# Kernel tuning notes

Measured on AMD Instinct MI355X. Metric: run time of the kernel, lower is better.

Reference implementation:

```python
import jax, jax.numpy as jnp
import numpy as np

B_, L_, D_ = 8, 2048, 1024
ED = 2 * D_          # d_inner (expand=2)
N_ = D_ // 16        # d_state = 64
R_ = -(-D_ // 16)    # dt_rank = ceil(d_model/16) = 64
K_ = 4               # d_conv
NL = 3               # number of mamba layers
NC = 2               # num_classes
STD = 0.02


def setup_inputs() -> dict:
    key = jax.random.key(0)
    ks = jax.random.split(key, 8)
    # Standard Mamba init: A_log = log(1..N) broadcast over channels
    A_log = jnp.log(jnp.tile(jnp.arange(1, N_ + 1, dtype=jnp.float32), (NL, ED, 1)))
    return {
        "x": jax.random.normal(ks[0], (B_, L_, D_), jnp.float32),
        "W_in": jax.random.normal(ks[1], (NL, 2 * ED, D_), jnp.float32) * STD,
        "conv_w": jax.random.normal(ks[2], (NL, ED, 1, K_), jnp.float32) * STD,
        "conv_b": jnp.zeros((NL, ED), jnp.float32),
        "W_x": jax.random.normal(ks[3], (NL, R_ + 2 * N_, ED), jnp.float32) * STD,
        "W_dt": jax.random.normal(ks[4], (NL, ED, R_), jnp.float32) * STD,
        "b_dt": jnp.zeros((NL, ED), jnp.float32),
        "A_log": A_log,
        "D_p": jnp.ones((NL, ED), jnp.float32),
        "W_out": jax.random.normal(ks[5], (NL, D_, ED), jnp.float32) * STD,
        "norm_w": jnp.ones((NL, D_), jnp.float32),
        "W_head": jax.random.normal(ks[6], (NC, D_), jnp.float32) * STD,
        "b_head": jnp.zeros((NC,), jnp.float32),
    }


def _silu(x):
    return x * jax.nn.sigmoid(x)


def _rmsnorm(x, w, eps=1e-5):
    return x * jax.lax.rsqrt(jnp.mean(x * x, axis=-1, keepdims=True) + eps) * w


def _mamba_block(x, Wi, cw, cb, Wx, Wdt, bdt, Alog, Dp, Wo):
    B, L, D = x.shape
    xz = x @ Wi.T                              # (B, L, 2*ED)
    xp, z = jnp.split(xz, 2, axis=-1)          # each (B, L, ED)
    # causal depthwise conv1d (kernel K_, left-pad K_-1)
    xc = jnp.transpose(xp, (0, 2, 1))          # (B, ED, L)
    xc = jax.lax.conv_general_dilated(
        xc, cw, window_strides=(1,), padding=[(K_ - 1, 0)],
        dimension_numbers=("NCH", "OIH", "NCH"), feature_group_count=ED,
    ) + cb[None, :, None]
    xp = _silu(jnp.transpose(xc, (0, 2, 1)))   # (B, L, ED)

    xdbl = xp @ Wx.T                           # (B, L, R + 2N)
    dt, Bm, Cm = jnp.split(xdbl, [R_, R_ + N_], axis=-1)
    delta = jax.nn.softplus(dt @ Wdt.T + bdt)  # (B, L, ED)
    A = -jnp.exp(Alog)                         # (ED, N)

    def step(h, inp):
        d_t, B_t, C_t, x_t = inp               # (B,ED), (B,N), (B,N), (B,ED)
        h = jnp.exp(d_t[..., None] * A) * h + (d_t * x_t)[..., None] * B_t[:, None, :]
        y_t = jnp.einsum("ben,bn->be", h, C_t)
        return h, y_t

    h0 = jnp.zeros((B, ED, N_), x.dtype)
    xs = (jnp.moveaxis(delta, 1, 0), jnp.moveaxis(Bm, 1, 0),
          jnp.moveaxis(Cm, 1, 0), jnp.moveaxis(xp, 1, 0))
    _, ys = jax.lax.scan(step, h0, xs)         # ys: (L, B, ED)
    y = jnp.moveaxis(ys, 0, 1) + xp * Dp       # (B, L, ED)
    y = y * _silu(z)
    return y @ Wo.T                            # (B, L, D)


def reference(x, W_in, conv_w, conv_b, W_x, W_dt, b_dt, A_log, D_p, W_out,
              norm_w, W_head, b_head):
    for i in range(NL):
        z = _mamba_block(x, W_in[i], conv_w[i], conv_b[i], W_x[i], W_dt[i],
                         b_dt[i], A_log[i], D_p[i], W_out[i])
        x = _rmsnorm(z, norm_w[i]) + x         # dropout_rate=0 -> identity
    last = x[:, -1, :]                         # (B, D)
    return last @ W_head.T + b_head            # (B, NC)
```

## Files before the change

### kernel.cpp

```cpp
#include <hip/hip_runtime.h>
#include <math.h>

#define B_ 8
#define L_ 2048
#define D_ 1024
#define ED_ 2048
#define NL_ 3
#define NC_ 2
#define SCH_ 128
#define NCH_ (L_ / SCH_)
#define GSZ_ 16
#define NGR_ (SCH_ / GSZ_)

typedef unsigned short u16;
typedef unsigned int u32;
typedef __attribute__((ext_vector_type(8))) short short8;
typedef __attribute__((ext_vector_type(4))) float f32x4;

#define LOG2E_ 1.44269504088896f

__device__ __forceinline__ u16 f2b(float f) {
    u32 u = __float_as_uint(f);
    u = (u + 0x7FFFu + ((u >> 16) & 1u)) >> 16;
    return (u16)u;
}
__device__ __forceinline__ float b2f(u16 h) {
    return __uint_as_float(((u32)h) << 16);
}
__device__ __forceinline__ float fexp2(float x) {
#if __has_builtin(__builtin_amdgcn_exp2f)
    return __builtin_amdgcn_exp2f(x);
#else
    return exp2f(x);
#endif
}
__device__ __forceinline__ void cp16(const void* g, void* l) {
    __builtin_amdgcn_global_load_lds((const __attribute__((address_space(1))) u32*)g,
                                     (__attribute__((address_space(3))) u32*)l,
                                     16, 0, 0);
}

__global__ __launch_bounds__(256)
void cast_bf16(const float* __restrict__ in, u16* __restrict__ out, int n)
{
    int i = blockIdx.x * 256 + threadIdx.x;
    if (i < n) out[i] = f2b(in[i]);
}

__global__ __launch_bounds__(256)
void cast_dt(const float* __restrict__ xdbl, u16* __restrict__ dtb)
{
    int idx = blockIdx.x * 256 + threadIdx.x;
    int m = idx >> 6, r = idx & 63;
    dtb[idx] = f2b(xdbl[(size_t)m * 192 + r]);
}

template<int BM, int BN, int EPI>
__global__ __launch_bounds__(256)
void gemm_mfma(const u16* __restrict__ A, int lda,
               const u16* __restrict__ W, const float* __restrict__ bias,
               void* __restrict__ Cout, int ldc, int Kd)
{
    constexpr int WX = (BN == 128) ? 2 : ((BM == 128) ? 1 : 2);
    constexpr int WY = 4 / WX;
    constexpr int MI = (BM / WY) / 16;
    constexpr int NI = (BN / WX) / 16;

    __shared__ u16 As[BM * 32];
    __shared__ u16 Bs[BN * 32];

    const int tid  = threadIdx.x;
    const int wave = tid >> 6;
    const int lane = tid & 63;
    const int wy = wave / WX, wx = wave % WX;
    const int by = blockIdx.y * BM;
    const int bx = blockIdx.x * BN;
    const int lr = lane & 15;
    const int lk = (lane >> 4) * 8;

    f32x4 acc[MI][NI];
#pragma unroll
    for (int i = 0; i < MI; i++)
#pragma unroll
        for (int j = 0; j < NI; j++) acc[i][j] = (f32x4){0.f, 0.f, 0.f, 0.f};

    const u16* Ag0 = A + (size_t)(by + (tid >> 2)) * lda + (tid & 3) * 8;
    const u16* Bg0 = W + (size_t)(bx + (tid >> 2)) * Kd + (tid & 3) * 8;
    u16* ldsA0 = &As[wave * 512];
    u16* ldsB0 = &Bs[wave * 512];

    for (int kt = 0; kt < Kd; kt += 32) {
        __syncthreads();
        cp16(Ag0 + kt, ldsA0);
        if (BM == 128) cp16(Ag0 + (size_t)64 * lda + kt, ldsA0 + 2048);
        cp16(Bg0 + kt, ldsB0);
        if (BN == 128) cp16(Bg0 + (size_t)64 * Kd + kt, ldsB0 + 2048);
        __syncthreads();

        short8 af[MI], bf[NI];
#pragma unroll
        for (int mi = 0; mi < MI; mi++) {
            int m = wy * (MI * 16) + mi * 16 + lr;
            af[mi] = *(const short8*)&As[m * 32 + lk];
        }
#pragma unroll
        for (int ni = 0; ni < NI; ni++) {
            int n = wx * (NI * 16) + ni * 16 + lr;
            bf[ni] = *(const short8*)&Bs[n * 32 + lk];
        }
#pragma unroll
        for (int mi = 0; mi < MI; mi++)
#pragma unroll
            for (int ni = 0; ni < NI; ni++)
                acc[mi][ni] = __builtin_amdgcn_mfma_f32_16x16x32_bf16(
                    af[mi], bf[ni], acc[mi][ni], 0, 0, 0);
    }

#pragma unroll
    for (int mi = 0; mi < MI; mi++) {
#pragma unroll
        for (int ni = 0; ni < NI; ni++) {
            int col = bx + wx * (NI * 16) + ni * 16 + lr;
#pragma unroll
            for (int r = 0; r < 4; r++) {
                int row = by + wy * (MI * 16) + mi * 16 + (lane >> 4) * 4 + r;
                float v = acc[mi][ni][r];
                if (EPI == 2) {
                    v += bias[col];
                    v = (v > 20.f) ? v : log1pf(__expf(v));
                }
                if (EPI == 1)
                    ((u16*)Cout)[(size_t)row * ldc + col] = f2b(v);
                else
                    ((float*)Cout)[(size_t)row * ldc + col] = v;
            }
        }
    }
}

__global__ __launch_bounds__(256)
void conv_silu(const u16* __restrict__ xzb, const float* __restrict__ cw,
               const float* __restrict__ cb, u16* __restrict__ xpb)
{
    int idx = blockIdx.x * 256 + threadIdx.x;
    int e = idx & (ED_ - 1);
    int l = (idx >> 11) & (L_ - 1);
    int b = idx >> 22;
    const float w0 = cw[e * 4 + 0], w1 = cw[e * 4 + 1];
    const float w2 = cw[e * 4 + 2], w3 = cw[e * 4 + 3];
    const u16* base = xzb + (size_t)(b * L_) * 4096 + e;
    float x0 = (l >= 3) ? b2f(base[(size_t)(l - 3) * 4096]) : 0.f;
    float x1 = (l >= 2) ? b2f(base[(size_t)(l - 2) * 4096]) : 0.f;
    float x2 = (l >= 1) ? b2f(base[(size_t)(l - 1) * 4096]) : 0.f;
    float x3 = b2f(base[(size_t)l * 4096]);
    float v = cb[e] + w0 * x0 + w1 * x1 + w2 * x2 + w3 * x3;
    v = v / (1.f + __expf(-v));
    xpb[idx] = f2b(v);
}

struct SlotP { const char* p; int st; };

__device__ __forceinline__ SlotP p1_slot(int s, const float* xdbl, const float* delta,
                                         const u16* xpb, size_t rowBase, int e0)
{
    SlotP r;
    if (s < 256) {
        int l = s >> 4, f = (s & 15) * 4;
        r.p = (const char*)(xdbl + (rowBase + l) * 192 + 64 + f);
        r.st = 16 * 192 * 4;
    } else if (s < 384) {
        int ss = s - 256; int l = ss >> 3, f = (ss & 7) * 4;
        r.p = (const char*)(delta + (rowBase + l) * 2048 + e0 + f);
        r.st = 16 * 2048 * 4;
    } else {
        int ss = s - 384; int l = ss >> 2, q = ss & 3;
        r.p = (const char*)(xpb + (rowBase + l) * 2048 + e0 + q * 8);
        r.st = 16 * 2048 * 2;
    }
    return r;
}

__global__ __launch_bounds__(512)
void scan_pass1(const float* __restrict__ delta, const float* __restrict__ xdbl,
                const u16* __restrict__ xpb, const float* __restrict__ A_log,
                float* __restrict__ hbuf, float* __restrict__ sumd)
{
    __shared__ __align__(16) char arena[2][7168];

    const int tid = threadIdx.x;
    const int wv = tid >> 6, ln = tid & 63;
    const int c = tid >> 4, j = tid & 15;
    const int b = blockIdx.z, ch = blockIdx.y;
    const int e0 = blockIdx.x << 5;
    const int e = e0 + c;
    const int l0 = ch * SCH_;
    const size_t rowBase = (size_t)(b * L_) + l0;

    const int s0 = wv * 56 + ln;
    SlotP sp0 = p1_slot(ln < 56 ? s0 : 0, xdbl, delta, xpb, rowBase, e0);
    const int d0 = s0 * 16;

    auto stage = [&](int gi) {
        char* a = (char*)arena[gi & 1];
        if (ln < 56) { cp16(sp0.p, a + d0); sp0.p += sp0.st; }
    };

    stage(0);

    float4 Al = *(const float4*)(A_log + (size_t)e * 64 + 4 * j);
    const float A0 = -__expf(Al.x) * LOG2E_, A1 = -__expf(Al.y) * LOG2E_;
    const float A2 = -__expf(Al.z) * LOG2E_, A3 = -__expf(Al.w) * LOG2E_;

    float h0 = 0.f, h1 = 0.f, h2 = 0.f, h3 = 0.f, sd = 0.f;

    for (int g = 0; g < NGR_; ++g) {
        if (g + 1 < NGR_) {
            stage(g + 1);
            asm volatile("s_waitcnt vmcnt(1)" ::: "memory");
        } else {
            asm volatile("s_waitcnt vmcnt(0)" ::: "memory");
        }
        __builtin_amdgcn_s_barrier();
        const char* bufp = (const char*)arena[g & 1];
#pragma unroll
        for (int t = 0; t < GSZ_; ++t) {
            float  dv = *(const float*)(bufp + 4096 + t * 128 + c * 4);
            float  xv = b2f(*(const u16*)(bufp + 6144 + t * 64 + c * 2));
            float4 Bv = *(const float4*)(bufp + t * 256 + j * 16);
            float dx = dv * xv;
            h0 = fexp2(dv * A0) * h0 + dx * Bv.x;
            h1 = fexp2(dv * A1) * h1 + dx * Bv.y;
            h2 = fexp2(dv * A2) * h2 + dx * Bv.z;
            h3 = fexp2(dv * A3) * h3 + dx * Bv.w;
            sd += dv;
        }
        __builtin_amdgcn_s_barrier();
    }

    size_t slot = (((size_t)(b * NCH_ + ch) * ED_) + e) * 64 + 4 * j;
    *(float4*)(hbuf + slot) = make_float4(h0, h1, h2, h3);
    if (j == 0) sumd[(size_t)(b * NCH_ + ch) * ED_ + e] = sd;
}

__global__ __launch_bounds__(256)
void scan_pass2(float* __restrict__ hbuf, const float* __restrict__ sumd,
                const float* __restrict__ A_log)
{
    int idx = blockIdx.x * 256 + threadIdx.x;
    int n = idx & 63;
    int e = (idx >> 6) & (ED_ - 1);
    int b = idx >> 17;
    float A = -__expf(A_log[e * 64 + n]) * LOG2E_;
    float h = 0.f;
#pragma unroll
    for (int c = 0; c < NCH_; ++c) {
        size_t slot = (((size_t)(b * NCH_ + c) * ED_) + e) * 64 + n;
        float v = 0.f, sd = 0.f;
        if (c < NCH_ - 1) {
            v  = hbuf[slot];
            sd = sumd[(size_t)(b * NCH_ + c) * ED_ + e];
        }
        hbuf[slot] = h;
        if (c < NCH_ - 1) h = fexp2(A * sd) * h + v;
    }
}

__device__ __forceinline__ SlotP p3_slot(int s, const float* xdbl, const float* delta,
                                         const u16* xpb, const u16* xzb,
                                         size_t rowBase, int e0)
{
    SlotP r;
    if (s < 512) {
        int cc = s >> 8;
        int l = (s >> 4) & 15, f = (s & 15) * 4;
        r.p = (const char*)(xdbl + (rowBase + l) * 192 + 64 + cc * 64 + f);
        r.st = 16 * 192 * 4;
    } else if (s < 640) {
        int ss = s - 512; int l = ss >> 3, f = (ss & 7) * 4;
        r.p = (const char*)(delta + (rowBase + l) * 2048 + e0 + f);
        r.st = 16 * 2048 * 4;
    } else if (s < 704) {
        int ss = s - 640; int l = ss >> 2, q = ss & 3;
        r.p = (const char*)(xpb + (rowBase + l) * 2048 + e0 + q * 8);
        r.st = 16 * 2048 * 2;
    } else {
        int ss = s - 704; int l = ss >> 2, q = ss & 3;
        r.p = (const char*)(xzb + (rowBase + l) * 4096 + 2048 + e0 + q * 8);
        r.st = 16 * 4096 * 2;
    }
    return r;
}

__global__ __launch_bounds__(512)
void scan_pass3(const float* __restrict__ delta, const float* __restrict__ xdbl,
                const u16* __restrict__ xzb, u16* __restrict__ xpb,
                const float* __restrict__ A_log, const float* __restrict__ Dp,
                const float* __restrict__ hbuf)
{
    __shared__ __align__(16) char arena[2][12288];

    const int tid = threadIdx.x;
    const int wv = tid >> 6, ln = tid & 63;
    const int c = tid >> 4, j = tid & 15;
    const int b = blockIdx.z, ch = blockIdx.y;
    const int e0 = blockIdx.x << 5;
    const int e = e0 + c;
    const int l0 = ch * SCH_;
    const size_t rowBase = (size_t)(b * L_) + l0;

    const int s0 = wv * 96 + ln;
    SlotP sp0 = p3_slot(s0, xdbl, delta, xpb, xzb, rowBase, e0);
    SlotP sp1 = p3_slot(ln < 32 ? s0 + 64 : s0, xdbl, delta, xpb, xzb, rowBase, e0);
    const int d0 = s0 * 16, d1 = d0 + 1024;

    auto stage = [&](int gi) {
        char* a = (char*)arena[gi & 1];
        cp16(sp0.p, a + d0); sp0.p += sp0.st;
        if (ln < 32) { cp16(sp1.p, a + d1); sp1.p += sp1.st; }
    };

    stage(0);

    float4 Al = *(const float4*)(A_log + (size_t)e * 64 + 4 * j);
    const float A0 = -__expf(Al.x) * LOG2E_, A1 = -__expf(Al.y) * LOG2E_;
    const float A2 = -__expf(Al.z) * LOG2E_, A3 = -__expf(Al.w) * LOG2E_;
    const float dpe = Dp[e];

    size_t slot = (((size_t)(b * NCH_ + ch) * ED_) + e) * 64 + 4 * j;
    float4 hi = *(const float4*)(hbuf + slot);
    float h0 = hi.x, h1 = hi.y, h2 = hi.z, h3 = hi.w;

    for (int g = 0; g < NGR_; ++g) {
        if (g + 1 < NGR_) {
            stage(g + 1);
            asm volatile("s_waitcnt vmcnt(2)" ::: "memory");
        } else {
            asm volatile("s_waitcnt vmcnt(0)" ::: "memory");
        }
        __builtin_amdgcn_s_barrier();
        const char* bufp = (const char*)arena[g & 1];

        float yreg = 0.f;
#pragma unroll
        for (int t = 0; t < GSZ_; ++t) {
            float  dv = *(const float*)(bufp + 8192 + t * 128 + c * 4);
            float  xv = b2f(*(const u16*)(bufp + 10240 + t * 64 + c * 2));
            float4 Bv = *(const float4*)(bufp + t * 256 + j * 16);
            float4 Cv = *(const float4*)(bufp + 4096 + t * 256 + j * 16);
            float dx = dv * xv;
            h0 = fexp2(dv * A0) * h0 + dx * Bv.x;
            h1 = fexp2(dv * A1) * h1 + dx * Bv.y;
            h2 = fexp2(dv * A2) * h2 + dx * Bv.z;
            h3 = fexp2(dv * A3) * h3 + dx * Bv.w;

            float acc = h0 * Cv.x + h1 * Cv.y + h2 * Cv.z + h3 * Cv.w;
            acc += __shfl_xor(acc, 1); acc += __shfl_xor(acc, 2);
            acc += __shfl_xor(acc, 4); acc += __shfl_xor(acc, 8);
            float yv = acc + xv * dpe;
            if (j == t) yreg = yv;
        }
        {
            float zv = b2f(*(const u16*)(bufp + 11264 + j * 64 + c * 2));
            float sz = zv / (1.f + __expf(-zv));
            xpb[(rowBase + g * 16 + j) * 2048 + e] = f2b(yreg * sz);
        }
        __builtin_amdgcn_s_barrier();
    }
}

__global__ __launch_bounds__(256)
void rmsnorm_res(const float* __restrict__ t, const float* __restrict__ nw,
                 float* __restrict__ x, u16* __restrict__ xb)
{
    const int row = blockIdx.x;
    const int tid = threadIdx.x;
    const float* tr = t + (size_t)row * D_;
    float* xr = x + (size_t)row * D_;
    u16* xbr = xb + (size_t)row * D_;
    float4 v = *(const float4*)(tr + tid * 4);
    float ss = v.x * v.x + v.y * v.y + v.z * v.z + v.w * v.w;
#pragma unroll
    for (int m = 1; m < 64; m <<= 1) ss += __shfl_xor(ss, m);
    __shared__ float red[4];
    if ((tid & 63) == 0) red[tid >> 6] = ss;
    __syncthreads();
    float tot = red[0] + red[1] + red[2] + red[3];
    float scale = rsqrtf(tot * (1.f / (float)D_) + 1e-5f);
    float4 w = *(const float4*)(nw + tid * 4);
    float4 xo = *(const float4*)(xr + tid * 4);
    xo.x += v.x * scale * w.x;
    xo.y += v.y * scale * w.y;
    xo.z += v.z * scale * w.z;
    xo.w += v.w * scale * w.w;
    *(float4*)(xr + tid * 4) = xo;
    ushort4 hb;
    hb.x = f2b(xo.x); hb.y = f2b(xo.y); hb.z = f2b(xo.z); hb.w = f2b(xo.w);
    *(ushort4*)(xbr + tid * 4) = hb;
}

__global__ __launch_bounds__(256)
void head_kernel(const float* __restrict__ x, const float* __restrict__ Wh,
                 const float* __restrict__ bh, float* __restrict__ out)
{
    const int b = blockIdx.x >> 1, c = blockIdx.x & 1;
    const int tid = threadIdx.x;
    const float* xr = x + (size_t)(b * L_ + (L_ - 1)) * D_;
    const float* wr = Wh + c * D_;
    float4 xv = *(const float4*)(xr + tid * 4);
    float4 wv = *(const float4*)(wr + tid * 4);
    float s = xv.x * wv.x + xv.y * wv.y + xv.z * wv.z + xv.w * wv.w;
#pragma unroll
    for (int m = 1; m < 64; m <<= 1) s += __shfl_xor(s, m);
    __shared__ float red[4];
    if ((tid & 63) == 0) red[tid >> 6] = s;
    __syncthreads();
    if (tid == 0) out[b * 2 + c] = red[0] + red[1] + red[2] + red[3] + bh[c];
}

extern "C" void kernel_launch(void* const* d_in, const int* in_sizes, int n_in,
                              void* d_out, int out_size, void* d_ws, size_t ws_size,
                              hipStream_t stream)
{
    const float* x_in   = (const float*)d_in[0];
    const float* W_in   = (const float*)d_in[1];
    const float* conv_w = (const float*)d_in[2];
    const float* conv_b = (const float*)d_in[3];
    const float* W_x    = (const float*)d_in[4];
    const float* W_dt   = (const float*)d_in[5];
    const float* b_dt   = (const float*)d_in[6];
    const float* A_log  = (const float*)d_in[7];
    const float* D_p    = (const float*)d_in[8];
    const float* W_out  = (const float*)d_in[9];
    const float* norm_w = (const float*)d_in[10];
    const float* W_head = (const float*)d_in[11];
    const float* b_head = (const float*)d_in[12];
    float* out = (float*)d_out;

    const size_t nWi = (size_t)NL_ * 2 * ED_ * D_;
    const size_t nWx = (size_t)NL_ * 192 * ED_;
    const size_t nWo = (size_t)NL_ * D_ * ED_;
    const size_t nWd = (size_t)NL_ * ED_ * 64;
    u16* Wi_b = (u16*)d_ws;
    u16* Wx_b = Wi_b + nWi;
    u16* Wo_b = Wx_b + nWx;
    u16* Wd_b = Wo_b + nWo;
    size_t wbytes = ((nWi + nWx + nWo + nWd) * 2 + 255) & ~(size_t)255;
    char* gb = (char*)d_ws + wbytes;
    size_t usable = ws_size - wbytes;

    cast_bf16<<<(int)(nWi / 256), 256, 0, stream>>>(W_in, Wi_b, (int)nWi);
    cast_bf16<<<(int)(nWx / 256), 256, 0, stream>>>(W_x,  Wx_b, (int)nWx);
    cast_bf16<<<(int)(nWo / 256), 256, 0, stream>>>(W_out, Wo_b, (int)nWo);
    cast_bf16<<<(int)(nWd / 256), 256, 0, stream>>>(W_dt,  Wd_b, (int)nWd);

    const size_t perB = (size_t)L_ * (D_ * 4 + 192 * 4 + ED_ * 4 + 4096 * 2 + ED_ * 2)
                      + (size_t)NCH_ * ED_ * 64 * 4 + (size_t)NCH_ * ED_ * 4
                      + (size_t)L_ * 64 * 2;
    int G = 8;
    while (G > 1 && (size_t)G * perB > usable) G >>= 1;
    const int M = G * L_;

    float* x_cur = (float*)gb;
    float* xdbl  = x_cur + (size_t)M * D_;
    float* delta = xdbl + (size_t)M * 192;
    u16*   x_b   = (u16*)delta;
    u16*   xz_b  = (u16*)(delta + (size_t)M * ED_);
    u16*   xps_b = xz_b + (size_t)M * 4096;
    float* hbuf  = (float*)(xps_b + (size_t)M * ED_);
    float* sumd  = hbuf + (size_t)G * NCH_ * ED_ * 64;
    u16*   dtb   = (u16*)(sumd + (size_t)G * NCH_ * ED_);
    float* out_t = (float*)xz_b;

    for (int g0 = 0; g0 < B_; g0 += G) {
        const float* xg = x_in + (size_t)g0 * L_ * D_;
        hipMemcpyAsync(x_cur, xg, (size_t)M * D_ * sizeof(float),
                       hipMemcpyDeviceToDevice, stream);
        cast_bf16<<<(M * D_) / 256, 256, 0, stream>>>(xg, x_b, M * D_);

        for (int i = 0; i < NL_; ++i) {
            gemm_mfma<128, 128, 1><<<dim3(4096 / 128, M / 128), 256, 0, stream>>>(
                x_b, D_, Wi_b + (size_t)i * 2 * ED_ * D_, nullptr, xz_b, 4096, D_);
            conv_silu<<<(M * ED_) / 256, 256, 0, stream>>>(
                xz_b, conv_w + (size_t)i * ED_ * 4, conv_b + (size_t)i * ED_, xps_b);
            gemm_mfma<64, 64, 0><<<dim3(192 / 64, M / 64), 256, 0, stream>>>(
                xps_b, ED_, Wx_b + (size_t)i * 192 * ED_, nullptr, xdbl, 192, ED_);
            cast_dt<<<(M * 64) / 256, 256, 0, stream>>>(xdbl, dtb);
            gemm_mfma<64, 64, 2><<<dim3(ED_ / 64, M / 64), 256, 0, stream>>>(
                dtb, 64, Wd_b + (size_t)i * ED_ * 64, b_dt + (size_t)i * ED_,
                delta, ED_, 64);
            scan_pass1<<<dim3(ED_ / 32, NCH_ - 1, G), 512, 0, stream>>>(
                delta, xdbl, xps_b, A_log + (size_t)i * ED_ * 64, hbuf, sumd);
            scan_pass2<<<G * 512, 256, 0, stream>>>(
                hbuf, sumd, A_log + (size_t)i * ED_ * 64);
            scan_pass3<<<dim3(ED_ / 32, NCH_, G), 512, 0, stream>>>(
                delta, xdbl, xz_b, xps_b,
                A_log + (size_t)i * ED_ * 64, D_p + (size_t)i * ED_, hbuf);
            gemm_mfma<64, 128, 0><<<dim3(D_ / 128, M / 64), 256, 0, stream>>>(
                xps_b, ED_, Wo_b + (size_t)i * D_ * ED_, nullptr, out_t, D_, ED_);
            rmsnorm_res<<<M, 256, 0, stream>>>(out_t, norm_w + (size_t)i * D_,
                                               x_cur, x_b);
        }
        head_kernel<<<G * NC_, 256, 0, stream>>>(x_cur, W_head, b_head,
                                                 out + (size_t)g0 * NC_);
    }
}
```

Baseline: 5.230 ms.

## Pack delta, x and z into interleaved 8-byte records; batch y reduction in scan

The delta GEMM epilogue now writes one 8-byte record per (row, channel) holding fp32 delta plus the bf16 x and z values, so both scan passes stage a single contiguous stream instead of three strided ones. In pass 3 the per-timestep 16-lane shuffle reduction of C·h is replaced by a recursive-halving transpose-reduce over a 16-element register array, which cuts the shuffle count. The cost is an extra read of xps and xz in the GEMM epilogue, a larger delta buffer, and more registers held in pass 3.

Result: faster. 4.661 ms (-10.9%).

```diff
diff --git a/kernel.cpp b/kernel.cpp
--- a/kernel.cpp
+++ b/kernel.cpp
@@ -59,7 +59,8 @@
 __global__ __launch_bounds__(256)
 void gemm_mfma(const u16* __restrict__ A, int lda,
                const u16* __restrict__ W, const float* __restrict__ bias,
-               void* __restrict__ Cout, int ldc, int Kd)
+               void* __restrict__ Cout, int ldc, int Kd,
+               const u16* __restrict__ xq, const u16* __restrict__ zq)
 {
     constexpr int WX = (BN == 128) ? 2 : ((BM == 128) ? 1 : 2);
     constexpr int WY = 4 / WX;
@@ -128,11 +129,17 @@
                 if (EPI == 2) {
                     v += bias[col];
                     v = (v > 20.f) ? v : log1pf(__expf(v));
+                    u16 xv = xq[(size_t)row * ED_ + col];
+                    u16 zv = zq[(size_t)row * 4096 + 2048 + col];
+                    uint2 pkv;
+                    pkv.x = __float_as_uint(v);
+                    pkv.y = (u32)xv | ((u32)zv << 16);
+                    ((uint2*)Cout)[(size_t)row * ldc + col] = pkv;
+                } else if (EPI == 1) {
+                    ((u16*)Cout)[(size_t)row * ldc + col] = f2b(v);
+                } else {
+                    ((float*)Cout)[(size_t)row * ldc + col] = v;
                 }
-                if (EPI == 1)
-                    ((u16*)Cout)[(size_t)row * ldc + col] = f2b(v);
-                else
-                    ((float*)Cout)[(size_t)row * ldc + col] = v;
             }
         }
     }
@@ -160,32 +167,28 @@
 
 struct SlotP { const char* p; int st; };
 
-__device__ __forceinline__ SlotP p1_slot(int s, const float* xdbl, const float* delta,
-                                         const u16* xpb, size_t rowBase, int e0)
+__device__ __forceinline__ SlotP p1_slot(int s, const float* xdbl, const char* pkc,
+                                         size_t rowBase, int e0)
 {
     SlotP r;
     if (s < 256) {
         int l = s >> 4, f = (s & 15) * 4;
         r.p = (const char*)(xdbl + (rowBase + l) * 192 + 64 + f);
         r.st = 16 * 192 * 4;
-    } else if (s < 384) {
-        int ss = s - 256; int l = ss >> 3, f = (ss & 7) * 4;
-        r.p = (const char*)(delta + (rowBase + l) * 2048 + e0 + f);
-        r.st = 16 * 2048 * 4;
     } else {
-        int ss = s - 384; int l = ss >> 2, q = ss & 3;
-        r.p = (const char*)(xpb + (rowBase + l) * 2048 + e0 + q * 8);
-        r.st = 16 * 2048 * 2;
+        int ss = s - 256; int l = ss >> 4, f = (ss & 15) * 16;
+        r.p = pkc + ((rowBase + l) * ED_ + e0) * 8 + f;
+        r.st = 16 * ED_ * 8;
     }
     return r;
 }
 
 __global__ __launch_bounds__(512)
-void scan_pass1(const float* __restrict__ delta, const float* __restrict__ xdbl,
-                const u16* __restrict__ xpb, const float* __restrict__ A_log,
+void scan_pass1(const char* __restrict__ pkc, const float* __restrict__ xdbl,
+                const float* __restrict__ A_log,
                 float* __restrict__ hbuf, float* __restrict__ sumd)
 {
-    __shared__ __align__(16) char arena[2][7168];
+    __shared__ __align__(16) char arena[2][8192];
 
     const int tid = threadIdx.x;
     const int wv = tid >> 6, ln = tid & 63;
@@ -196,13 +199,13 @@
     const int l0 = ch * SCH_;
     const size_t rowBase = (size_t)(b * L_) + l0;
 
-    const int s0 = wv * 56 + ln;
-    SlotP sp0 = p1_slot(ln < 56 ? s0 : 0, xdbl, delta, xpb, rowBase, e0);
+    const int s0 = wv * 64 + ln;
+    SlotP sp0 = p1_slot(s0, xdbl, pkc, rowBase, e0);
     const int d0 = s0 * 16;
 
     auto stage = [&](int gi) {
         char* a = (char*)arena[gi & 1];
-        if (ln < 56) { cp16(sp0.p, a + d0); sp0.p += sp0.st; }
+        cp16(sp0.p, a + d0); sp0.p += sp0.st;
     };
 
     stage(0);
@@ -224,8 +227,9 @@
         const char* bufp = (const char*)arena[g & 1];
 #pragma unroll
         for (int t = 0; t < GSZ_; ++t) {
-            float  dv = *(const float*)(bufp + 4096 + t * 128 + c * 4);
-            float  xv = b2f(*(const u16*)(bufp + 6144 + t * 64 + c * 2));
+            uint2 pkv = *(const uint2*)(bufp + 4096 + t * 256 + c * 8);
+            float dv = __uint_as_float(pkv.x);
+            float xv = b2f((u16)(pkv.y & 0xFFFFu));
             float4 Bv = *(const float4*)(bufp + t * 256 + j * 16);
             float dx = dv * xv;
             h0 = fexp2(dv * A0) * h0 + dx * Bv.x;
@@ -265,8 +269,7 @@
     }
 }
 
-__device__ __forceinline__ SlotP p3_slot(int s, const float* xdbl, const float* delta,
-                                         const u16* xpb, const u16* xzb,
+__device__ __forceinline__ SlotP p3_slot(int s, const float* xdbl, const char* pkc,
                                          size_t rowBase, int e0)
 {
     SlotP r;
@@ -275,25 +278,17 @@
         int l = (s >> 4) & 15, f = (s & 15) * 4;
         r.p = (const char*)(xdbl + (rowBase + l) * 192 + 64 + cc * 64 + f);
         r.st = 16 * 192 * 4;
-    } else if (s < 640) {
-        int ss = s - 512; int l = ss >> 3, f = (ss & 7) * 4;
-        r.p = (const char*)(delta + (rowBase + l) * 2048 + e0 + f);
-        r.st = 16 * 2048 * 4;
-    } else if (s < 704) {
-        int ss = s - 640; int l = ss >> 2, q = ss & 3;
-        r.p = (const char*)(xpb + (rowBase + l) * 2048 + e0 + q * 8);
-        r.st = 16 * 2048 * 2;
     } else {
-        int ss = s - 704; int l = ss >> 2, q = ss & 3;
-        r.p = (const char*)(xzb + (rowBase + l) * 4096 + 2048 + e0 + q * 8);
-        r.st = 16 * 4096 * 2;
+        int ss = s - 512; int l = ss >> 4, f = (ss & 15) * 16;
+        r.p = pkc + ((rowBase + l) * ED_ + e0) * 8 + f;
+        r.st = 16 * ED_ * 8;
     }
     return r;
 }
 
 __global__ __launch_bounds__(512)
-void scan_pass3(const float* __restrict__ delta, const float* __restrict__ xdbl,
-                const u16* __restrict__ xzb, u16* __restrict__ xpb,
+void scan_pass3(const char* __restrict__ pkc, const float* __restrict__ xdbl,
+                u16* __restrict__ xpb,
                 const float* __restrict__ A_log, const float* __restrict__ Dp,
                 const float* __restrict__ hbuf)
 {
@@ -309,8 +304,8 @@
     const size_t rowBase = (size_t)(b * L_) + l0;
 
     const int s0 = wv * 96 + ln;
-    SlotP sp0 = p3_slot(s0, xdbl, delta, xpb, xzb, rowBase, e0);
-    SlotP sp1 = p3_slot(ln < 32 ? s0 + 64 : s0, xdbl, delta, xpb, xzb, rowBase, e0);
+    SlotP sp0 = p3_slot(s0, xdbl, pkc, rowBase, e0);
+    SlotP sp1 = p3_slot(ln < 32 ? s0 + 64 : s0, xdbl, pkc, rowBase, e0);
     const int d0 = s0 * 16, d1 = d0 + 1024;
 
     auto stage = [&](int gi) {
@@ -340,11 +335,12 @@
         __builtin_amdgcn_s_barrier();
         const char* bufp = (const char*)arena[g & 1];
 
-        float yreg = 0.f;
+        float P[GSZ_];
 #pragma unroll
         for (int t = 0; t < GSZ_; ++t) {
-            float  dv = *(const float*)(bufp + 8192 + t * 128 + c * 4);
-            float  xv = b2f(*(const u16*)(bufp + 10240 + t * 64 + c * 2));
+            uint2 pkv = *(const uint2*)(bufp + 8192 + t * 256 + c * 8);
+            float dv = __uint_as_float(pkv.x);
+            float xv = b2f((u16)(pkv.y & 0xFFFFu));
             float4 Bv = *(const float4*)(bufp + t * 256 + j * 16);
             float4 Cv = *(const float4*)(bufp + 4096 + t * 256 + j * 16);
             float dx = dv * xv;
@@ -352,17 +348,44 @@
             h1 = fexp2(dv * A1) * h1 + dx * Bv.y;
             h2 = fexp2(dv * A2) * h2 + dx * Bv.z;
             h3 = fexp2(dv * A3) * h3 + dx * Bv.w;
-
-            float acc = h0 * Cv.x + h1 * Cv.y + h2 * Cv.z + h3 * Cv.w;
-            acc += __shfl_xor(acc, 1); acc += __shfl_xor(acc, 2);
-            acc += __shfl_xor(acc, 4); acc += __shfl_xor(acc, 8);
-            float yv = acc + xv * dpe;
-            if (j == t) yreg = yv;
+            P[t] = h0 * Cv.x + h1 * Cv.y + h2 * Cv.z + h3 * Cv.w;
+        }
+
+#pragma unroll
+        for (int i = 0; i < 8; ++i) {
+            float a = P[i], bb = P[i + 8];
+            float keep = (j & 8) ? bb : a;
+            float send = (j & 8) ? a : bb;
+            P[i] = keep + __shfl_xor(send, 8);
+        }
+#pragma unroll
+        for (int i = 0; i < 4; ++i) {
+            float a = P[i], bb = P[i + 4];
+            float keep = (j & 4) ? bb : a;
+            float send = (j & 4) ? a : bb;
+            P[i] = keep + __shfl_xor(send, 4);
+        }
+#pragma unroll
+        for (int i = 0; i < 2; ++i) {
+            float a = P[i], bb = P[i + 2];
+            float keep = (j & 2) ? bb : a;
+            float send = (j & 2) ? a : bb;
+            P[i] = keep + __shfl_xor(send, 2);
         }
         {
-            float zv = b2f(*(const u16*)(bufp + 11264 + j * 64 + c * 2));
-            float sz = zv / (1.f + __expf(-zv));
-            xpb[(rowBase + g * 16 + j) * 2048 + e] = f2b(yreg * sz);
+            float a = P[0], bb = P[1];
+            float keep = (j & 1) ? bb : a;
+            float send = (j & 1) ? a : bb;
+            P[0] = keep + __shfl_xor(send, 1);
+        }
+
+        {
+            uint2 pj = *(const uint2*)(bufp + 8192 + j * 256 + c * 8);
+            float xj = b2f((u16)(pj.y & 0xFFFFu));
+            float zj = b2f((u16)(pj.y >> 16));
+            float yv = P[0] + xj * dpe;
+            float sz = zj / (1.f + __expf(-zj));
+            xpb[(rowBase + g * 16 + j) * 2048 + e] = f2b(yv * sz);
         }
         __builtin_amdgcn_s_barrier();
     }
@@ -453,7 +476,7 @@
     cast_bf16<<<(int)(nWo / 256), 256, 0, stream>>>(W_out, Wo_b, (int)nWo);
     cast_bf16<<<(int)(nWd / 256), 256, 0, stream>>>(W_dt,  Wd_b, (int)nWd);
 
-    const size_t perB = (size_t)L_ * (D_ * 4 + 192 * 4 + ED_ * 4 + 4096 * 2 + ED_ * 2)
+    const size_t perB = (size_t)L_ * (D_ * 4 + 192 * 4 + ED_ * 8 + 4096 * 2 + ED_ * 2)
                       + (size_t)NCH_ * ED_ * 64 * 4 + (size_t)NCH_ * ED_ * 4
                       + (size_t)L_ * 64 * 2;
     int G = 8;
@@ -462,9 +485,9 @@
 
     float* x_cur = (float*)gb;
     float* xdbl  = x_cur + (size_t)M * D_;
-    float* delta = xdbl + (size_t)M * 192;
-    u16*   x_b   = (u16*)delta;
-    u16*   xz_b  = (u16*)(delta + (size_t)M * ED_);
+    uint2* pk    = (uint2*)(xdbl + (size_t)M * 192);
+    u16*   x_b   = (u16*)pk;
+    u16*   xz_b  = (u16*)(pk + (size_t)M * ED_);
     u16*   xps_b = xz_b + (size_t)M * 4096;
     float* hbuf  = (float*)(xps_b + (size_t)M * ED_);
     float* sumd  = hbuf + (size_t)G * NCH_ * ED_ * 64;
@@ -479,24 +502,27 @@
 
         for (int i = 0; i < NL_; ++i) {
             gemm_mfma<128, 128, 1><<<dim3(4096 / 128, M / 128), 256, 0, stream>>>(
-                x_b, D_, Wi_b + (size_t)i * 2 * ED_ * D_, nullptr, xz_b, 4096, D_);
+                x_b, D_, Wi_b + (size_t)i * 2 * ED_ * D_, nullptr, xz_b, 4096, D_,
+                nullptr, nullptr);
             conv_silu<<<(M * ED_) / 256, 256, 0, stream>>>(
                 xz_b, conv_w + (size_t)i * ED_ * 4, conv_b + (size_t)i * ED_, xps_b);
             gemm_mfma<64, 64, 0><<<dim3(192 / 64, M / 64), 256, 0, stream>>>(
-                xps_b, ED_, Wx_b + (size_t)i * 192 * ED_, nullptr, xdbl, 192, ED_);
+                xps_b, ED_, Wx_b + (size_t)i * 192 * ED_, nullptr, xdbl, 192, ED_,
+                nullptr, nullptr);
             cast_dt<<<(M * 64) / 256, 256, 0, stream>>>(xdbl, dtb);
             gemm_mfma<64, 64, 2><<<dim3(ED_ / 64, M / 64), 256, 0, stream>>>(
                 dtb, 64, Wd_b + (size_t)i * ED_ * 64, b_dt + (size_t)i * ED_,
-                delta, ED_, 64);
+                pk, ED_, 64, xps_b, xz_b);
             scan_pass1<<<dim3(ED_ / 32, NCH_ - 1, G), 512, 0, stream>>>(
-                delta, xdbl, xps_b, A_log + (size_t)i * ED_ * 64, hbuf, sumd);
+                (const char*)pk, xdbl, A_log + (size_t)i * ED_ * 64, hbuf, sumd);
             scan_pass2<<<G * 512, 256, 0, stream>>>(
                 hbuf, sumd, A_log + (size_t)i * ED_ * 64);
             scan_pass3<<<dim3(ED_ / 32, NCH_, G), 512, 0, stream>>>(
-                delta, xdbl, xz_b, xps_b,
+                (const char*)pk, xdbl, xps_b,
                 A_log + (size_t)i * ED_ * 64, D_p + (size_t)i * ED_, hbuf);
             gemm_mfma<64, 128, 0><<<dim3(D_ / 128, M / 64), 256, 0, stream>>>(
-                xps_b, ED_, Wo_b + (size_t)i * D_ * ED_, nullptr, out_t, D_, ED_);
+                xps_b, ED_, Wo_b + (size_t)i * D_ * ED_, nullptr, out_t, D_, ED_,
+                nullptr, nullptr);
             rmsnorm_res<<<M, 256, 0, stream>>>(out_t, norm_w + (size_t)i * D_,
                                                x_cur, x_b);
         }
```
